# Performance work log

Hardware: AMD Instinct MI355X
Metric: run time of the kernel (lower is better)

The kernel has to match this reference:

```python
import jax, jax.numpy as jnp
import numpy as np

U = 100000  # num_users
I = 100000  # num_items
D = 64      # dims
L = 50      # seq_L


def setup_inputs() -> dict:
    key = jax.random.key(0)
    ks = jax.random.split(key, 12)
    B, T = 4096, 100
    inp = {
        "user_ids": jax.random.randint(ks[0], (B,), 0, U),
        "item_seq_ids": jax.random.randint(ks[1], (B, L), 0, I),
        "target_item_ids": jax.random.randint(ks[2], (B, T), 0, I),
        # embedding tables (normal init)
        "user_table": jax.random.normal(ks[3], (U, D), jnp.float32) * 0.01,
        "item_table": jax.random.normal(ks[4], (I, D), jnp.float32) * 0.01,
        "W2_table": jax.random.normal(ks[5], (I, D), jnp.float32) * 0.01,
        "b2_table": jnp.zeros((I, 1), jnp.float32),
        # feature gates: Linear(dims, dims), he_uniform weight, zero bias
        "fg_item_W": jax.random.uniform(ks[6], (D, D), jnp.float32, -1.0, 1.0) * np.sqrt(6.0 / D),
        "fg_item_b": jnp.zeros((D,), jnp.float32),
        "fg_user_W": jax.random.uniform(ks[7], (D, D), jnp.float32, -1.0, 1.0) * np.sqrt(6.0 / D),
        "fg_user_b": jnp.zeros((D,), jnp.float32),
        # instance gates: xavier_uniform
        "inst_gate_item": jax.random.uniform(ks[8], (D, 1), jnp.float32, -1.0, 1.0) * np.sqrt(6.0 / (D + 1)),
        "inst_gate_user": jax.random.uniform(ks[9], (D, L), jnp.float32, -1.0, 1.0) * np.sqrt(6.0 / (D + L)),
    }
    return inp


def _forward_user(user_emb, item_embs, fg_item_W, fg_item_b, fg_user_W, fg_user_b,
                  inst_gate_item, inst_gate_user):
    # user_emb: [B,D], item_embs: [B,L,D]
    gate = jax.nn.sigmoid(
        item_embs @ fg_item_W.T + fg_item_b
        + (user_emb @ fg_user_W.T + fg_user_b)[:, None, :]
    )  # [B,L,D]
    gated = item_embs * gate  # [B,L,D]
    term1 = jnp.einsum("bld,d->bl", gated, inst_gate_item[:, 0])
    term2 = user_emb @ inst_gate_user  # [B,L]
    inst = jax.nn.sigmoid(term1 + term2)  # [B,L]
    union = jnp.sum(gated * inst[:, :, None], axis=1)  # [B,D]
    union = union / jnp.sum(inst, axis=1, keepdims=True)
    return union


def reference(user_ids, item_seq_ids, target_item_ids, user_table, item_table,
              W2_table, b2_table, fg_item_W, fg_item_b, fg_user_W, fg_user_b,
              inst_gate_item, inst_gate_user):
    item_embs = item_table[item_seq_ids]      # [B,L,D]
    user_emb = user_table[user_ids]           # [B,D]
    union = _forward_user(user_emb, item_embs, fg_item_W, fg_item_b,
                          fg_user_W, fg_user_b, inst_gate_item, inst_gate_user)
    w2 = W2_table[target_item_ids]            # [B,T,D]
    b2 = b2_table[target_item_ids][..., 0]    # [B,T]
    res = b2 + jnp.einsum("btd,bd->bt", w2, user_emb)
    res = res + jnp.einsum("bd,btd->bt", union, w2)
    # rel_score: bmm(item_embs, w2^T) summed over L == contract item_embs summed over L with w2
    res = res + jnp.einsum("bd,btd->bt", jnp.sum(item_embs, axis=1), w2)
    return res
```

## Files before the change

kernel.cpp:

```cpp
#include <hip/hip_runtime.h>

#define DD 64
#define LL 50
#define NB 4096
#define NT 100
#define ES 68

typedef __attribute__((ext_vector_type(8))) __bf16 bf16x8;
typedef __attribute__((ext_vector_type(4))) float f32x4;

__device__ __forceinline__ float sigmoidf_(float x) {
    return 1.0f / (1.0f + __expf(-x));
}
__device__ __forceinline__ unsigned pack_bf16(float hi, float lo) {
    union { float f; unsigned u; } a, b;
    a.f = hi; b.f = lo;
    return ((a.u + 0x8000u) & 0xffff0000u) | ((b.u + 0x8000u) >> 16);
}
__device__ __forceinline__ bf16x8 cvt8(const float* f) {
    uint4 r;
    r.x = pack_bf16(f[1], f[0]);
    r.y = pack_bf16(f[3], f[2]);
    r.z = pack_bf16(f[5], f[4]);
    r.w = pack_bf16(f[7], f[6]);
    return __builtin_bit_cast(bf16x8, r);
}

__global__ __launch_bounds__(256) void hgn_fused(
    const int* __restrict__ user_ids,
    const int* __restrict__ item_seq_ids,
    const int* __restrict__ target_ids,
    const float* __restrict__ user_table,
    const float* __restrict__ item_table,
    const float* __restrict__ W2_table,
    const float* __restrict__ b2_table,
    const float* __restrict__ fg_item_W,
    const float* __restrict__ fg_item_b,
    const float* __restrict__ fg_user_W,
    const float* __restrict__ fg_user_b,
    const float* __restrict__ igi,
    const float* __restrict__ igu,
    float* __restrict__ out)
{
    const int b = blockIdx.x;
    const int tid = threadIdx.x;
    const int w = tid >> 6, lane = tid & 63;
    const int c = lane & 15, q = lane >> 4;

    __shared__ float sE[LL * ES];
    __shared__ float sufg[DD];
    __shared__ float st2[DD];
    __shared__ float spart[4 * DD];
    __shared__ float ssump[4 * DD];
    __shared__ float sisum[4];
    __shared__ float sv[DD];

    const int* iid = item_seq_ids + b * LL;
    const int uid = user_ids[b];

    for (int s = tid; s < LL * 8; s += 256) {
        const int l = s >> 3, ch = s & 7;
        const float* src = item_table + (size_t)iid[l] * DD + ch * 8;
        float4 v0 = *(const float4*)src;
        float4 v1 = *(const float4*)(src + 4);
        *(float4*)&sE[l * ES + ch * 8] = v0;
        *(float4*)&sE[l * ES + ch * 8 + 4] = v1;
    }

    if (w == 0) {
        const int d = lane;
        float acc = fg_user_b[d] + fg_item_b[d];
#pragma unroll
        for (int k4 = 0; k4 < 16; k4++) {
            float4 wr = *(const float4*)(fg_user_W + d * DD + k4 * 4);
            float4 uk = *(const float4*)(user_table + (size_t)uid * DD + k4 * 4);
            acc += wr.x * uk.x + wr.y * uk.y + wr.z * uk.z + wr.w * uk.w;
        }
        sufg[d] = acc;
    } else if (w == 1) {
        const int l = lane;
        float acc = 0.f;
        if (l < LL) {
#pragma unroll 16
            for (int k = 0; k < DD; k++)
                acc += user_table[(size_t)uid * DD + k] * igu[k * LL + l];
        }
        st2[lane] = acc;
    }

    bf16x8 wb[4][2];
#pragma unroll
    for (int ni = 0; ni < 4; ni++) {
#pragma unroll
        for (int kf = 0; kf < 2; kf++) {
            float tmp[8];
            const float* src = fg_item_W + (ni * 16 + c) * DD + kf * 32 + q * 8;
            *(float4*)&tmp[0] = *(const float4*)src;
            *(float4*)&tmp[4] = *(const float4*)(src + 4);
            wb[ni][kf] = cvt8(tmp);
        }
    }
    bf16x8 ea[2];
    {
        float tmp[16];
        const int la = w * 16 + c;
        if (la < LL) {
            const float* src = item_table + (size_t)iid[la] * DD;
            *(float4*)&tmp[0]  = *(const float4*)(src + q * 8);
            *(float4*)&tmp[4]  = *(const float4*)(src + q * 8 + 4);
            *(float4*)&tmp[8]  = *(const float4*)(src + 32 + q * 8);
            *(float4*)&tmp[12] = *(const float4*)(src + 32 + q * 8 + 4);
        } else {
#pragma unroll
            for (int i = 0; i < 16; i++) tmp[i] = 0.f;
        }
        ea[0] = cvt8(tmp);
        ea[1] = cvt8(tmp + 8);
    }

    f32x4 acc[4];
#pragma unroll
    for (int ni = 0; ni < 4; ni++) {
        f32x4 a = {0.f, 0.f, 0.f, 0.f};
        a = __builtin_amdgcn_mfma_f32_16x16x32_bf16(ea[0], wb[ni][0], a, 0, 0, 0);
        a = __builtin_amdgcn_mfma_f32_16x16x32_bf16(ea[1], wb[ni][1], a, 0, 0, 0);
        acc[ni] = a;
    }
    __syncthreads();

    float ufg4[4], igi4[4];
#pragma unroll
    for (int ni = 0; ni < 4; ni++) {
        ufg4[ni] = sufg[ni * 16 + c];
        igi4[ni] = igi[ni * 16 + c];
    }

    float gated[4][4];
    float inst_r[4];
    float unum[4] = {0.f, 0.f, 0.f, 0.f};
    float sip[4]  = {0.f, 0.f, 0.f, 0.f};
#pragma unroll
    for (int reg = 0; reg < 4; reg++) {
        const int l = w * 16 + q * 4 + reg;
        const int lc = (l < LL) ? l : 0;
        const float lm = (l < LL) ? 1.f : 0.f;
        float t1 = 0.f;
#pragma unroll
        for (int ni = 0; ni < 4; ni++) {
            const float e = sE[lc * ES + ni * 16 + c] * lm;
            const float g = sigmoidf_(acc[ni][reg] + ufg4[ni]);
            const float gd = e * g;
            gated[reg][ni] = gd;
            t1 += gd * igi4[ni];
            sip[ni] += e;
        }
        t1 += __shfl_xor(t1, 1); t1 += __shfl_xor(t1, 2);
        t1 += __shfl_xor(t1, 4); t1 += __shfl_xor(t1, 8);
        inst_r[reg] = (l < LL) ? sigmoidf_(t1 + st2[lc]) : 0.f;
    }

    float isum = inst_r[0] + inst_r[1] + inst_r[2] + inst_r[3];
#pragma unroll
    for (int ni = 0; ni < 4; ni++)
#pragma unroll
        for (int reg = 0; reg < 4; reg++)
            unum[ni] += gated[reg][ni] * inst_r[reg];

#pragma unroll
    for (int ni = 0; ni < 4; ni++) {
        unum[ni] += __shfl_xor(unum[ni], 16); unum[ni] += __shfl_xor(unum[ni], 32);
        sip[ni]  += __shfl_xor(sip[ni], 16);  sip[ni]  += __shfl_xor(sip[ni], 32);
    }
    isum += __shfl_xor(isum, 16); isum += __shfl_xor(isum, 32);

    const float un = (q == 0) ? unum[0] : (q == 1) ? unum[1] : (q == 2) ? unum[2] : unum[3];
    const float si = (q == 0) ? sip[0]  : (q == 1) ? sip[1]  : (q == 2) ? sip[2]  : sip[3];
    spart[w * DD + lane] = un;
    ssump[w * DD + lane] = si;
    if (lane == 0) sisum[w] = isum;
    __syncthreads();

    if (w == 0) {
        const int d = lane;
        const float num = spart[d] + spart[DD + d] + spart[2 * DD + d] + spart[3 * DD + d];
        const float ss  = ssump[d] + ssump[DD + d] + ssump[2 * DD + d] + ssump[3 * DD + d];
        const float den = sisum[0] + sisum[1] + sisum[2] + sisum[3];
        sv[d] = user_table[(size_t)uid * DD + d] + num / den + ss;
    }
    __syncthreads();

    const int j = tid & 7, g = tid >> 3;
    float vreg[8];
#pragma unroll
    for (int i = 0; i < 8; i++) vreg[i] = sv[j * 8 + i];

#pragma unroll
    for (int it = 0; it < 4; it++) {
        const int t = it * 32 + g;
        if (t < NT) {
            const int id = target_ids[b * NT + t];
            const float* wrow = W2_table + (size_t)id * DD + j * 8;
            float4 w0 = *(const float4*)(wrow);
            float4 w1 = *(const float4*)(wrow + 4);
            float s = w0.x * vreg[0] + w0.y * vreg[1] + w0.z * vreg[2] + w0.w * vreg[3]
                    + w1.x * vreg[4] + w1.y * vreg[5] + w1.z * vreg[6] + w1.w * vreg[7];
            s += __shfl_xor(s, 1);
            s += __shfl_xor(s, 2);
            s += __shfl_xor(s, 4);
            if (j == 0) out[b * NT + t] = s + b2_table[id];
        }
    }
}

extern "C" void kernel_launch(void* const* d_in, const int* in_sizes, int n_in,
                              void* d_out, int out_size, void* d_ws, size_t ws_size,
                              hipStream_t stream)
{
    const int* user_ids        = (const int*)d_in[0];
    const int* item_seq_ids    = (const int*)d_in[1];
    const int* target_item_ids = (const int*)d_in[2];
    const float* user_tab      = (const float*)d_in[3];
    const float* item_tab      = (const float*)d_in[4];
    const float* W2_tab        = (const float*)d_in[5];
    const float* b2_tab        = (const float*)d_in[6];
    const float* fg_item_W     = (const float*)d_in[7];
    const float* fg_item_b     = (const float*)d_in[8];
    const float* fg_user_W     = (const float*)d_in[9];
    const float* fg_user_b     = (const float*)d_in[10];
    const float* igi           = (const float*)d_in[11];
    const float* igu           = (const float*)d_in[12];
    float* out = (float*)d_out;

    hgn_fused<<<NB, 256, 0, stream>>>(user_ids, item_seq_ids, target_item_ids,
                                      user_tab, item_tab, W2_tab, b2_tab,
                                      fg_item_W, fg_item_b, fg_user_W, fg_user_b,
                                      igi, igu, out);
}
```

Measured before the change: 186.2 us.

## Split fused kernel into user-projection, union, and scoring kernels via workspace

Splits the single fused per-batch kernel into three launches. The first batches user-side projections (fg_user and inst_gate_user) across 16 users with MFMA. The second computes the union vector for four batch rows per block, with one wave per row and bf16 item embeddings staged in shared memory. The third does the W2 target scoring. This removes the serial per-block user GEMV and the idle waves, and raises parallelism in each phase, at the cost of extra launches and workspace round-trips through global memory. The fused path is kept as a fallback when the workspace is too small.

```diff
diff --git a/kernel.cpp b/kernel.cpp
--- a/kernel.cpp
+++ b/kernel.cpp
@@ -12,35 +12,241 @@
 __device__ __forceinline__ float sigmoidf_(float x) {
     return 1.0f / (1.0f + __expf(-x));
 }
+__device__ __forceinline__ float b2f(unsigned short h) {
+    union { unsigned int u; float f; } v; v.u = ((unsigned int)h) << 16; return v.f;
+}
 __device__ __forceinline__ unsigned pack_bf16(float hi, float lo) {
     union { float f; unsigned u; } a, b;
     a.f = hi; b.f = lo;
     return ((a.u + 0x8000u) & 0xffff0000u) | ((b.u + 0x8000u) >> 16);
 }
-__device__ __forceinline__ bf16x8 cvt8(const float* f) {
+__device__ __forceinline__ uint4 cvt8u(const float* f) {
     uint4 r;
     r.x = pack_bf16(f[1], f[0]);
     r.y = pack_bf16(f[3], f[2]);
     r.z = pack_bf16(f[5], f[4]);
     r.w = pack_bf16(f[7], f[6]);
-    return __builtin_bit_cast(bf16x8, r);
+    return r;
+}
+__device__ __forceinline__ bf16x8 cvt8(const float* f) {
+    return __builtin_bit_cast(bf16x8, cvt8u(f));
+}
+
+__global__ __launch_bounds__(64) void k0_user(
+    const int* __restrict__ uid_g, const float* __restrict__ user_table,
+    const float* __restrict__ Wu, const float* __restrict__ bu,
+    const float* __restrict__ bi, const float* __restrict__ igu,
+    float* __restrict__ ufg_ws, float* __restrict__ t2_ws)
+{
+    const int lane = threadIdx.x;
+    const int c = lane & 15, q = lane >> 4;
+    const int uid = uid_g[blockIdx.x * 16 + c];
+    const float* urow = user_table + (size_t)uid * DD;
+
+    bf16x8 af[2];
+#pragma unroll
+    for (int kf = 0; kf < 2; kf++) {
+        float tmp[8];
+        *(float4*)&tmp[0] = *(const float4*)(urow + kf * 32 + q * 8);
+        *(float4*)&tmp[4] = *(const float4*)(urow + kf * 32 + q * 8 + 4);
+        af[kf] = cvt8(tmp);
+    }
+
+#pragma unroll
+    for (int ni = 0; ni < 8; ni++) {
+        f32x4 a = {0.f, 0.f, 0.f, 0.f};
+#pragma unroll
+        for (int kf = 0; kf < 2; kf++) {
+            const int k0 = kf * 32 + q * 8;
+            float tmp[8];
+            if (ni < 4) {
+                const float* src = Wu + (ni * 16 + c) * DD + k0;
+                *(float4*)&tmp[0] = *(const float4*)src;
+                *(float4*)&tmp[4] = *(const float4*)(src + 4);
+            } else {
+                const int l = ni * 16 + c - 64;
+#pragma unroll
+                for (int j = 0; j < 8; j++)
+                    tmp[j] = (l < LL) ? igu[(k0 + j) * LL + l] : 0.f;
+            }
+            a = __builtin_amdgcn_mfma_f32_16x16x32_bf16(af[kf], cvt8(tmp), a, 0, 0, 0);
+        }
+        const int n = ni * 16 + c;
+#pragma unroll
+        for (int reg = 0; reg < 4; reg++) {
+            const int bo = blockIdx.x * 16 + q * 4 + reg;
+            if (n < DD)           ufg_ws[bo * DD + n] = a[reg] + bu[n] + bi[n];
+            else if (n < DD + LL) t2_ws[bo * DD + (n - DD)] = a[reg];
+        }
+    }
+}
+
+__global__ __launch_bounds__(256) void k1_union(
+    const int* __restrict__ uid_g, const int* __restrict__ iid_g,
+    const float* __restrict__ user_table, const float* __restrict__ item_table,
+    const float* __restrict__ Wi, const float* __restrict__ igi,
+    const float* __restrict__ ufg_ws, const float* __restrict__ t2_ws,
+    float* __restrict__ v_ws)
+{
+    const int tid = threadIdx.x;
+    const int w = tid >> 6, lane = tid & 63;
+    const int c = lane & 15, q = lane >> 4;
+    const int b = blockIdx.x * 4 + w;
+
+    __shared__ unsigned short sE[4][LL][72];
+    __shared__ unsigned short sW[DD][72];
+
+    {
+        const int n = tid >> 2, ch = tid & 3;
+        float tmp[16];
+        const float* src = Wi + n * DD + ch * 16;
+        *(float4*)&tmp[0]  = *(const float4*)(src);
+        *(float4*)&tmp[4]  = *(const float4*)(src + 4);
+        *(float4*)&tmp[8]  = *(const float4*)(src + 8);
+        *(float4*)&tmp[12] = *(const float4*)(src + 12);
+        *(uint4*)&sW[n][ch * 16]     = cvt8u(tmp);
+        *(uint4*)&sW[n][ch * 16 + 8] = cvt8u(tmp + 8);
+    }
+
+    const int* iid = iid_g + b * LL;
+    bf16x8 ea[4][2];
+#pragma unroll
+    for (int mi = 0; mi < 4; mi++) {
+        const int l = mi * 16 + c;
+        if (l < LL) {
+            const float* src = item_table + (size_t)iid[l] * DD;
+#pragma unroll
+            for (int kf = 0; kf < 2; kf++) {
+                float tmp[8];
+                *(float4*)&tmp[0] = *(const float4*)(src + kf * 32 + q * 8);
+                *(float4*)&tmp[4] = *(const float4*)(src + kf * 32 + q * 8 + 4);
+                uint4 p = cvt8u(tmp);
+                ea[mi][kf] = __builtin_bit_cast(bf16x8, p);
+                *(uint4*)&sE[w][l][kf * 32 + q * 8] = p;
+            }
+        } else {
+            uint4 z = {0u, 0u, 0u, 0u};
+            ea[mi][0] = __builtin_bit_cast(bf16x8, z);
+            ea[mi][1] = __builtin_bit_cast(bf16x8, z);
+        }
+    }
+    __syncthreads();
+
+    bf16x8 wb[4][2];
+#pragma unroll
+    for (int ni = 0; ni < 4; ni++)
+#pragma unroll
+        for (int kf = 0; kf < 2; kf++)
+            wb[ni][kf] = __builtin_bit_cast(bf16x8,
+                *(const uint4*)&sW[ni * 16 + c][kf * 32 + q * 8]);
+
+    float ufg4[4], igi4[4];
+#pragma unroll
+    for (int ni = 0; ni < 4; ni++) {
+        ufg4[ni] = ufg_ws[b * DD + ni * 16 + c];
+        igi4[ni] = igi[ni * 16 + c];
+    }
+
+    float unum[4] = {0.f, 0.f, 0.f, 0.f};
+    float sip[4]  = {0.f, 0.f, 0.f, 0.f};
+    float isum = 0.f;
+
+#pragma unroll
+    for (int mi = 0; mi < 4; mi++) {
+        f32x4 acc[4];
+#pragma unroll
+        for (int ni = 0; ni < 4; ni++) {
+            f32x4 a = {0.f, 0.f, 0.f, 0.f};
+            a = __builtin_amdgcn_mfma_f32_16x16x32_bf16(ea[mi][0], wb[ni][0], a, 0, 0, 0);
+            a = __builtin_amdgcn_mfma_f32_16x16x32_bf16(ea[mi][1], wb[ni][1], a, 0, 0, 0);
+            acc[ni] = a;
+        }
+        float gated[4][4], inst_r[4];
+#pragma unroll
+        for (int reg = 0; reg < 4; reg++) {
+            const int l = mi * 16 + q * 4 + reg;
+            const int valid = (l < LL);
+            const int lc = valid ? l : 0;
+            const float lm = valid ? 1.f : 0.f;
+            float t1 = 0.f;
+#pragma unroll
+            for (int ni = 0; ni < 4; ni++) {
+                const float e = b2f(sE[w][lc][ni * 16 + c]) * lm;
+                const float g = sigmoidf_(acc[ni][reg] + ufg4[ni]);
+                const float gd = e * g;
+                gated[reg][ni] = gd;
+                t1 += gd * igi4[ni];
+                sip[ni] += e;
+            }
+            t1 += __shfl_xor(t1, 1); t1 += __shfl_xor(t1, 2);
+            t1 += __shfl_xor(t1, 4); t1 += __shfl_xor(t1, 8);
+            inst_r[reg] = valid ? sigmoidf_(t1 + t2_ws[b * DD + lc]) : 0.f;
+        }
+#pragma unroll
+        for (int reg = 0; reg < 4; reg++) {
+            isum += inst_r[reg];
+#pragma unroll
+            for (int ni = 0; ni < 4; ni++)
+                unum[ni] += gated[reg][ni] * inst_r[reg];
+        }
+    }
+
+#pragma unroll
+    for (int ni = 0; ni < 4; ni++) {
+        unum[ni] += __shfl_xor(unum[ni], 16); unum[ni] += __shfl_xor(unum[ni], 32);
+        sip[ni]  += __shfl_xor(sip[ni], 16);  sip[ni]  += __shfl_xor(sip[ni], 32);
+    }
+    isum += __shfl_xor(isum, 16); isum += __shfl_xor(isum, 32);
+
+    const float un = (q == 0) ? unum[0] : (q == 1) ? unum[1] : (q == 2) ? unum[2] : unum[3];
+    const float si = (q == 0) ? sip[0]  : (q == 1) ? sip[1]  : (q == 2) ? sip[2]  : sip[3];
+    const int uid = uid_g[b];
+    const float u = user_table[(size_t)uid * DD + lane];
+    v_ws[b * DD + lane] = u + un / isum + si;
+}
+
+__global__ __launch_bounds__(256) void k2_score(
+    const int* __restrict__ tgt_g, const float* __restrict__ W2,
+    const float* __restrict__ b2, const float* __restrict__ v_ws,
+    float* __restrict__ out)
+{
+    const int b = blockIdx.x;
+    const int tid = threadIdx.x;
+    __shared__ float sv[DD];
+    if (tid < DD) sv[tid] = v_ws[b * DD + tid];
+    __syncthreads();
+
+    const int j = tid & 7, g = tid >> 3;
+    float vr[8];
+#pragma unroll
+    for (int i = 0; i < 8; i++) vr[i] = sv[j * 8 + i];
+
+#pragma unroll
+    for (int it = 0; it < 4; it++) {
+        const int t = it * 32 + g;
+        if (t < NT) {
+            const int id = tgt_g[b * NT + t];
+            const float* wrow = W2 + (size_t)id * DD + j * 8;
+            float4 w0 = *(const float4*)(wrow);
+            float4 w1 = *(const float4*)(wrow + 4);
+            float s = w0.x * vr[0] + w0.y * vr[1] + w0.z * vr[2] + w0.w * vr[3]
+                    + w1.x * vr[4] + w1.y * vr[5] + w1.z * vr[6] + w1.w * vr[7];
+            s += __shfl_xor(s, 1);
+            s += __shfl_xor(s, 2);
+            s += __shfl_xor(s, 4);
+            if (j == 0) out[b * NT + t] = s + b2[id];
+        }
+    }
 }
 
 __global__ __launch_bounds__(256) void hgn_fused(
-    const int* __restrict__ user_ids,
-    const int* __restrict__ item_seq_ids,
-    const int* __restrict__ target_ids,
-    const float* __restrict__ user_table,
-    const float* __restrict__ item_table,
-    const float* __restrict__ W2_table,
-    const float* __restrict__ b2_table,
-    const float* __restrict__ fg_item_W,
-    const float* __restrict__ fg_item_b,
-    const float* __restrict__ fg_user_W,
-    const float* __restrict__ fg_user_b,
-    const float* __restrict__ igi,
-    const float* __restrict__ igu,
-    float* __restrict__ out)
+    const int* __restrict__ user_ids, const int* __restrict__ item_seq_ids,
+    const int* __restrict__ target_ids, const float* __restrict__ user_table,
+    const float* __restrict__ item_table, const float* __restrict__ W2_table,
+    const float* __restrict__ b2_table, const float* __restrict__ fg_item_W,
+    const float* __restrict__ fg_item_b, const float* __restrict__ fg_user_W,
+    const float* __restrict__ fg_user_b, const float* __restrict__ igi,
+    const float* __restrict__ igu, float* __restrict__ out)
 {
     const int b = blockIdx.x;
     const int tid = threadIdx.x;
@@ -90,7 +296,7 @@
 
     bf16x8 wb[4][2];
 #pragma unroll
-    for (int ni = 0; ni < 4; ni++) {
+    for (int ni = 0; ni < 4; ni++)
 #pragma unroll
         for (int kf = 0; kf < 2; kf++) {
             float tmp[8];
@@ -99,7 +305,6 @@
             *(float4*)&tmp[4] = *(const float4*)(src + 4);
             wb[ni][kf] = cvt8(tmp);
         }
-    }
     bf16x8 ea[2];
     {
         float tmp[16];
@@ -135,8 +340,7 @@
         igi4[ni] = igi[ni * 16 + c];
     }
 
-    float gated[4][4];
-    float inst_r[4];
+    float gated[4][4], inst_r[4];
     float unum[4] = {0.f, 0.f, 0.f, 0.f};
     float sip[4]  = {0.f, 0.f, 0.f, 0.f};
 #pragma unroll
@@ -190,10 +394,9 @@
     __syncthreads();
 
     const int j = tid & 7, g = tid >> 3;
-    float vreg[8];
-#pragma unroll
-    for (int i = 0; i < 8; i++) vreg[i] = sv[j * 8 + i];
-
+    float vr[8];
+#pragma unroll
+    for (int i = 0; i < 8; i++) vr[i] = sv[j * 8 + i];
 #pragma unroll
     for (int it = 0; it < 4; it++) {
         const int t = it * 32 + g;
@@ -202,8 +405,8 @@
             const float* wrow = W2_table + (size_t)id * DD + j * 8;
             float4 w0 = *(const float4*)(wrow);
             float4 w1 = *(const float4*)(wrow + 4);
-            float s = w0.x * vreg[0] + w0.y * vreg[1] + w0.z * vreg[2] + w0.w * vreg[3]
-                    + w1.x * vreg[4] + w1.y * vreg[5] + w1.z * vreg[6] + w1.w * vreg[7];
+            float s = w0.x * vr[0] + w0.y * vr[1] + w0.z * vr[2] + w0.w * vr[3]
+                    + w1.x * vr[4] + w1.y * vr[5] + w1.z * vr[6] + w1.w * vr[7];
             s += __shfl_xor(s, 1);
             s += __shfl_xor(s, 2);
             s += __shfl_xor(s, 4);
@@ -231,8 +434,21 @@
     const float* igu           = (const float*)d_in[12];
     float* out = (float*)d_out;
 
-    hgn_fused<<<NB, 256, 0, stream>>>(user_ids, item_seq_ids, target_item_ids,
-                                      user_tab, item_tab, W2_tab, b2_tab,
-                                      fg_item_W, fg_item_b, fg_user_W, fg_user_b,
-                                      igi, igu, out);
-}
+    const size_t need = (size_t)3 * NB * DD * sizeof(float);
+    if (ws_size >= need) {
+        float* ufg_ws = (float*)d_ws;
+        float* t2_ws  = ufg_ws + NB * DD;
+        float* v_ws   = t2_ws + NB * DD;
+        k0_user<<<NB / 16, 64, 0, stream>>>(user_ids, user_tab, fg_user_W,
+                                            fg_user_b, fg_item_b, igu, ufg_ws, t2_ws);
+        k1_union<<<NB / 4, 256, 0, stream>>>(user_ids, item_seq_ids, user_tab,
+                                             item_tab, fg_item_W, igi, ufg_ws,
+                                             t2_ws, v_ws);
+        k2_score<<<NB, 256, 0, stream>>>(target_item_ids, W2_tab, b2_tab, v_ws, out);
+    } else {
+        hgn_fused<<<NB, 256, 0, stream>>>(user_ids, item_seq_ids, target_item_ids,
+                                          user_tab, item_tab, W2_tab, b2_tab,
+                                          fg_item_W, fg_item_b, fg_user_W, fg_user_b,
+                                          igi, igu, out);
+    }
+}
```

Result: faster. 161.7 us (-13.2%).
